# Optimization experiments

Hardware: AMD Instinct MI355X
Metric: run time of the kernel (lower is better)

## Reference

```python
import jax, jax.numpy as jnp
import numpy as np
from jax import lax

LOOKBACK = 336
N_FEATURES = 164
HORIZON = 96
D_MODEL = 64
D_STATE = 16
D_CONV = 4
EXPAND = 2
D_INNER = EXPAND * D_MODEL  # 128
DT_RANK = (D_MODEL + 15) // 16  # 4
MLP_HIDDEN = 64
BATCH = 512


def setup_inputs() -> dict:
    key = jax.random.key(0)
    ks = jax.random.split(key, 20)
    f32 = jnp.float32
    inp = {}
    inp["x_raw"] = jax.random.normal(ks[0], (BATCH, LOOKBACK), f32)
    inp["x_features"] = jax.random.normal(ks[1], (BATCH, N_FEATURES), f32)
    # embed Linear(1, d_model)
    inp["embed_W"] = jax.random.normal(ks[2], (1, D_MODEL), f32) * 0.5
    inp["embed_b"] = jnp.zeros((D_MODEL,), f32)
    # Mamba params (mamba-ssm layout, stored as [in, out] for matmul)
    inp["in_W"] = jax.random.normal(ks[3], (D_MODEL, 2 * D_INNER), f32) * (1.0 / np.sqrt(D_MODEL))
    inp["conv_W"] = jax.random.normal(ks[4], (D_INNER, D_CONV), f32) * 0.3
    inp["conv_b"] = jnp.zeros((D_INNER,), f32)
    inp["xproj_W"] = jax.random.normal(ks[5], (D_INNER, DT_RANK + 2 * D_STATE), f32) * (1.0 / np.sqrt(D_INNER))
    inp["dt_W"] = jax.random.normal(ks[6], (DT_RANK, D_INNER), f32) * (1.0 / np.sqrt(DT_RANK))
    inp["dt_b"] = jax.random.uniform(ks[7], (D_INNER,), f32, -4.0, -2.0)  # softplus -> small dt
    # A_log init = log(arange(1..d_state)) broadcast over d_inner, as in mamba-ssm
    inp["A_log"] = jnp.log(jnp.broadcast_to(jnp.arange(1, D_STATE + 1, dtype=f32), (D_INNER, D_STATE)))
    inp["D"] = jnp.ones((D_INNER,), f32)
    inp["out_W"] = jax.random.normal(ks[8], (D_INNER, D_MODEL), f32) * (1.0 / np.sqrt(D_INNER))
    # MLP stream
    inp["mlp_W1"] = jax.random.normal(ks[9], (N_FEATURES, MLP_HIDDEN), f32) * (1.0 / np.sqrt(N_FEATURES))
    inp["mlp_b1"] = jnp.zeros((MLP_HIDDEN,), f32)
    inp["mlp_W2"] = jax.random.normal(ks[10], (MLP_HIDDEN, MLP_HIDDEN // 2), f32) * (1.0 / np.sqrt(MLP_HIDDEN))
    inp["mlp_b2"] = jnp.zeros((MLP_HIDDEN // 2,), f32)
    # prediction head
    fin = D_MODEL + MLP_HIDDEN // 2
    inp["head_W"] = jax.random.normal(ks[11], (fin, HORIZON), f32) * (1.0 / np.sqrt(fin))
    inp["head_b"] = jnp.zeros((HORIZON,), f32)
    return inp


def silu(x):
    return x * jax.nn.sigmoid(x)


def mamba_block(u, in_W, conv_W, conv_b, xproj_W, dt_W, dt_b, A_log, D, out_W):
    # u: [B, L, d_model]
    B_, L, _ = u.shape
    xz = u @ in_W                      # [B, L, 2*D_INNER]
    x, z = jnp.split(xz, 2, axis=-1)   # each [B, L, D_INNER]
    # causal depthwise conv1d (pad left d_conv-1), then SiLU
    xc = x.transpose(0, 2, 1)          # [B, D_INNER, L]
    kern = conv_W[:, None, :]          # [D_INNER, 1, K] (OIH)
    xc = lax.conv_general_dilated(xc, kern, window_strides=(1,),
                                  padding=[(D_CONV - 1, 0)],
                                  dimension_numbers=("NCH", "OIH", "NCH"),
                                  feature_group_count=D_INNER)
    xc = silu(xc + conv_b[None, :, None])
    x = xc.transpose(0, 2, 1)          # [B, L, D_INNER]
    # input-dependent SSM params
    x_dbl = x @ xproj_W                # [B, L, DT_RANK + 2*D_STATE]
    dt = x_dbl[..., :DT_RANK]
    Bm = x_dbl[..., DT_RANK:DT_RANK + D_STATE]          # [B, L, N]
    Cm = x_dbl[..., DT_RANK + D_STATE:]                 # [B, L, N]
    delta = jax.nn.softplus(dt @ dt_W + dt_b)           # [B, L, D_INNER]
    A = -jnp.exp(A_log)                                 # [D_INNER, N]

    # selective scan over time
    def step(h, inps):
        d_t, B_t, C_t, x_t = inps  # [B,Di], [B,N], [B,N], [B,Di]
        dA = jnp.exp(d_t[:, :, None] * A[None])              # [B, Di, N]
        dBx = (d_t * x_t)[:, :, None] * B_t[:, None, :]      # [B, Di, N]
        h = dA * h + dBx
        y_t = jnp.einsum("bdn,bn->bd", h, C_t)
        return h, y_t

    h0 = jnp.zeros((B_, D_INNER, D_STATE), u.dtype)
    seq = (delta.transpose(1, 0, 2), Bm.transpose(1, 0, 2),
           Cm.transpose(1, 0, 2), x.transpose(1, 0, 2))
    _, ys = lax.scan(step, h0, seq)        # ys: [L, B, D_INNER]
    y = ys.transpose(1, 0, 2) + x * D[None, None, :]
    y = y * silu(z)
    return y @ out_W                        # [B, L, d_model]


def reference(x_raw, x_features, embed_W, embed_b, in_W, conv_W, conv_b,
              xproj_W, dt_W, dt_b, A_log, D, out_W,
              mlp_W1, mlp_b1, mlp_W2, mlp_b2, head_W, head_b):
    # embed raw series: [B, L] -> [B, L, 1] -> [B, L, d_model]
    h = x_raw[..., None] @ embed_W + embed_b
    h = mamba_block(h, in_W, conv_W, conv_b, xproj_W, dt_W, dt_b, A_log, D, out_W)
    h_mamba_out = h[:, -1, :]                       # [B, d_model]
    h_mlp = jax.nn.relu(x_features @ mlp_W1 + mlp_b1) @ mlp_W2 + mlp_b2
    h_final = jnp.concatenate([h_mamba_out, h_mlp], axis=1)
    return h_final @ head_W + head_b                # [B, horizon]
```

## Files before the change

kernel.cpp:

```cpp
#include <hip/hip_runtime.h>
#include <math.h>

#define LOOKBACK 336
#define NFEAT    164
#define HORIZON  96
#define DMODEL   64
#define DSTATE   16
#define DINNER   128
#define MLPH     64
#define BATCH    512
#define XCP      132
#define NG       4
#define GSEG     84
#define CHK      12
#define NCH      7
#define HSTR     20

typedef float v2f __attribute__((ext_vector_type(2)));

__device__ __forceinline__ float fast_rcp(float x) { return __builtin_amdgcn_rcpf(x); }
__device__ __forceinline__ float silu_f(float x) {
    return x * fast_rcp(1.f + __expf(-x));
}

__global__ __launch_bounds__(512, 4) void mamba_one(
    const float* __restrict__ x_raw,   const float* __restrict__ x_features,
    const float* __restrict__ embed_W, const float* __restrict__ embed_b,
    const float* __restrict__ in_W,
    const float* __restrict__ conv_W,  const float* __restrict__ conv_b,
    const float* __restrict__ xproj_W, const float* __restrict__ dt_W,
    const float* __restrict__ dt_b,    const float* __restrict__ A_log,
    const float* __restrict__ Dvec,    const float* __restrict__ out_W,
    const float* __restrict__ mlp_W1,  const float* __restrict__ mlp_b1,
    const float* __restrict__ mlp_W2,  const float* __restrict__ mlp_b2,
    const float* __restrict__ head_W,  const float* __restrict__ head_b,
    float* __restrict__ out)
{
    __shared__ __align__(16) float xrl[344];
    __shared__ __align__(16) float xprojT[20*XCP];
    __shared__ __align__(16) float xcbuf[2][NG][CHK*XCP];
    __shared__ __align__(16) float Bsh[NG][CHK][DSTATE];
    __shared__ __align__(16) float dtraw[NG][CHK][4];
    __shared__ float xcl[DINNER], zsil[DINNER], Cl[DSTATE], yv[DINNER];
    __shared__ float hfin[96], mlph[MLPH];

    const int tid = threadIdx.x;
    const int b   = blockIdx.x;
    const int g   = tid >> 7;
    const int ch  = tid & 127;

    for (int i = tid; i < 339; i += 512)
        xrl[i] = (i >= 3) ? x_raw[b*LOOKBACK + i - 3] : 0.f;
    for (int idx = tid; idx < 20*DINNER; idx += 512) {
        int jj = idx >> 7, d = idx & 127;
        xprojT[jj*XCP + d] = xproj_W[d*36 + jj];
    }

    float w1 = 0.f, w0 = 0.f;
    for (int dm = 0; dm < DMODEL; ++dm) {
        float w = in_W[dm*(2*DINNER) + ch];
        w1 = fmaf(embed_W[dm], w, w1);
        w0 = fmaf(embed_b[dm], w, w0);
    }
    const float4 cw = *(const float4*)&conv_W[ch*4];
    const float  cb = conv_b[ch];
    const float dtw0 = dt_W[ch],       dtw1 = dt_W[128 + ch],
                dtw2 = dt_W[256 + ch], dtw3 = dt_W[384 + ch];
    const float dtb_r = dt_b[ch];
    bool structured = true;
    #pragma unroll
    for (int i = 0; i < 16; ++i) {
        float a = __expf(A_log[ch*DSTATE + i]);
        float ex = (float)(i + 1);
        structured = structured && (fabsf(a - ex) < 1e-3f * ex);
    }
    const bool sfast = __all(structured);

    const int a2jp  = tid / 24;
    const int a2rem = tid - a2jp*24;
    const int a2sub = a2rem / 12;
    const int a2tt  = a2rem - a2sub*12;
    const int cch    = (tid - 256) & 127;
    const int gfirst = (tid - 256) >> 7;
    __syncthreads();

    {
        float* xw = &xcbuf[0][g][0];
        const float* xr = &xrl[g*GSEG];
        if (g == 0) {
            for (int tt = 0; tt < CHK; ++tt) {
                float acc = cb;
                if (tt >= 3) acc = fmaf(fmaf(xr[tt],   w1, w0), cw.x, acc);
                if (tt >= 2) acc = fmaf(fmaf(xr[tt+1], w1, w0), cw.y, acc);
                if (tt >= 1) acc = fmaf(fmaf(xr[tt+2], w1, w0), cw.z, acc);
                acc = fmaf(fmaf(xr[tt+3], w1, w0), cw.w, acc);
                xw[tt*XCP + ch] = silu_f(acc);
            }
        } else {
            float e0 = fmaf(xr[0], w1, w0);
            float e1 = fmaf(xr[1], w1, w0);
            float e2 = fmaf(xr[2], w1, w0);
            #pragma unroll
            for (int tt = 0; tt < CHK; ++tt) {
                float e3 = fmaf(xr[tt+3], w1, w0);
                float acc = cb + e0*cw.x + e1*cw.y + e2*cw.z + e3*cw.w;
                xw[tt*XCP + ch] = silu_f(acc);
                e0 = e1; e1 = e2; e2 = e3;
            }
        }
    }
    __syncthreads();

    v2f h01={0,0},h23={0,0},h45={0,0},h67={0,0},
        h89={0,0},hAB={0,0},hCD={0,0},hEF={0,0};
    float dacc = 0.f;

    for (int c = 0; c < NCH; ++c) {
        const int buf = c & 1;

        if (tid < 240) {
            const int ga = a2sub*2, gb = a2sub*2 + 1;
            const int j0 = a2jp*2;
            const float* p0  = &xprojT[j0*XCP];
            const float* p1  = &xprojT[(j0+1)*XCP];
            const float* xra = &xcbuf[buf][ga][a2tt*XCP];
            const float* xrb = &xcbuf[buf][gb][a2tt*XCP];
            v2f a0a={0,0}, a1a={0,0}, a0b={0,0}, a1b={0,0};
            #pragma unroll 4
            for (int d = 0; d < DINNER; d += 4) {
                float4 q0 = *(const float4*)(p0 + d);
                float4 q1 = *(const float4*)(p1 + d);
                float4 xa = *(const float4*)(xra + d);
                float4 xb = *(const float4*)(xrb + d);
                v2f q0l={q0.x,q0.y}, q0h={q0.z,q0.w};
                v2f q1l={q1.x,q1.y}, q1h={q1.z,q1.w};
                v2f xal={xa.x,xa.y}, xah={xa.z,xa.w};
                v2f xbl={xb.x,xb.y}, xbh={xb.z,xb.w};
                a0a = __builtin_elementwise_fma(xal, q0l, a0a);
                a0a = __builtin_elementwise_fma(xah, q0h, a0a);
                a1a = __builtin_elementwise_fma(xal, q1l, a1a);
                a1a = __builtin_elementwise_fma(xah, q1h, a1a);
                a0b = __builtin_elementwise_fma(xbl, q0l, a0b);
                a0b = __builtin_elementwise_fma(xbh, q0h, a0b);
                a1b = __builtin_elementwise_fma(xbl, q1l, a1b);
                a1b = __builtin_elementwise_fma(xbh, q1h, a1b);
            }
            float r0a=a0a.x+a0a.y, r1a=a1a.x+a1a.y;
            float r0b=a0b.x+a0b.y, r1b=a1b.x+a1b.y;
            if (j0 < 4) {
                *(float2*)&dtraw[ga][a2tt][j0] = make_float2(r0a, r1a);
                *(float2*)&dtraw[gb][a2tt][j0] = make_float2(r0b, r1b);
            } else {
                *(float2*)&Bsh[ga][a2tt][j0-4] = make_float2(r0a, r1a);
                *(float2*)&Bsh[gb][a2tt][j0-4] = make_float2(r0b, r1b);
            }
        } else if (tid >= 256) {
            if (c + 1 < NCH) {
                #pragma unroll
                for (int q = 0; q < 2; ++q) {
                    const int gg = gfirst + q*2;
                    float* xw = &xcbuf[buf^1][gg][0];
                    const float* xr = &xrl[gg*GSEG + (c+1)*CHK];
                    float e0 = fmaf(xr[0], w1, w0);
                    float e1 = fmaf(xr[1], w1, w0);
                    float e2 = fmaf(xr[2], w1, w0);
                    float v = 0.f;
                    #pragma unroll
                    for (int tt = 0; tt < CHK; ++tt) {
                        float e3 = fmaf(xr[tt+3], w1, w0);
                        float acc = cb + e0*cw.x + e1*cw.y + e2*cw.z + e3*cw.w;
                        v = silu_f(acc);
                        xw[tt*XCP + cch] = v;
                        e0 = e1; e1 = e2; e2 = e3;
                    }
                    if (gg == NG-1 && c + 1 == NCH-1) xcl[cch] = v;
                }
            } else {
                if (tid < 384) {
                    const int c2 = tid - 256;
                    float a1 = 0.f, a0 = 0.f;
                    for (int dm = 0; dm < DMODEL; ++dm) {
                        float w = in_W[dm*(2*DINNER) + DINNER + c2];
                        a1 = fmaf(embed_W[dm], w, a1);
                        a0 = fmaf(embed_b[dm], w, a0);
                    }
                    zsil[c2] = silu_f(fmaf(xrl[338], a1, a0));
                } else if (tid < 448) {
                    const int lane = tid - 384;
                    const int n = lane & 15, q = lane >> 4;
                    float acc = 0.f;
                    for (int d = q*32; d < q*32 + 32; ++d)
                        acc = fmaf(xcl[d], xproj_W[d*36 + 20 + n], acc);
                    acc += __shfl_xor(acc, 16);
                    acc += __shfl_xor(acc, 32);
                    if (lane < 16) Cl[n] = acc;
                } else {
                    const int j = tid - 448;
                    const float* xf = x_features + b*NFEAT;
                    float acc = 0.f;
                    for (int f = 0; f < NFEAT; ++f)
                        acc = fmaf(xf[f], mlp_W1[f*MLPH + j], acc);
                    mlph[j] = fmaxf(acc + mlp_b1[j], 0.f);
                }
            }
        }
        __syncthreads();

        const float* xs = &xcbuf[buf][g][0];
        if (__builtin_expect(sfast, 1)) {
            #pragma unroll
            for (int tt = 0; tt < CHK; ++tt) {
                float4 dr = *(const float4*)&dtraw[g][tt][0];
                float dv = fmaf(dr.x, dtw0, fmaf(dr.y, dtw1,
                           fmaf(dr.z, dtw2, fmaf(dr.w, dtw3, dtb_r))));
                float e  = __expf(dv);
                float p  = 1.f + e;
                float r  = fast_rcp(p);
                float dl = (dv > 80.f) ? dv : __logf(p);
                dacc += dl;
                float ux = dl * xs[tt*XCP + ch];
                float4 B0 = *(const float4*)&Bsh[g][tt][0];
                float4 B1 = *(const float4*)&Bsh[g][tt][4];
                float4 B2 = *(const float4*)&Bsh[g][tt][8];
                float4 B3 = *(const float4*)&Bsh[g][tt][12];
                float r2 = r*r, r4 = r2*r2, r8 = r4*r4;
                v2f r2v = {r2, r2}, r4v = {r4, r4}, r8v = {r8, r8};
                v2f p01 = {r, r2};
                v2f p23 = p01*r2v;
                v2f p45 = p01*r4v, p67 = p23*r4v;
                v2f p89 = p01*r8v, pAB = p23*r8v, pCD = p45*r8v, pEF = p67*r8v;
                v2f uxv = {ux, ux};
                h01 = __builtin_elementwise_fma(p01, h01, uxv*(v2f){B0.x,B0.y});
                h23 = __builtin_elementwise_fma(p23, h23, uxv*(v2f){B0.z,B0.w});
                h45 = __builtin_elementwise_fma(p45, h45, uxv*(v2f){B1.x,B1.y});
                h67 = __builtin_elementwise_fma(p67, h67, uxv*(v2f){B1.z,B1.w});
                h89 = __builtin_elementwise_fma(p89, h89, uxv*(v2f){B2.x,B2.y});
                hAB = __builtin_elementwise_fma(pAB, hAB, uxv*(v2f){B2.z,B2.w});
                hCD = __builtin_elementwise_fma(pCD, hCD, uxv*(v2f){B3.x,B3.y});
                hEF = __builtin_elementwise_fma(pEF, hEF, uxv*(v2f){B3.z,B3.w});
            }
        } else {
            const float* Arow = A_log + ch*DSTATE;
            for (int tt = 0; tt < CHK; ++tt) {
                float4 dr = *(const float4*)&dtraw[g][tt][0];
                float dv = fmaf(dr.x, dtw0, fmaf(dr.y, dtw1,
                           fmaf(dr.z, dtw2, fmaf(dr.w, dtw3, dtb_r))));
                float e  = __expf(dv);
                float dl = (dv > 15.f) ? dv : __logf(1.f + e);
                dacc += dl;
                float ux = dl * xs[tt*XCP + ch];
                const float* Brow = &Bsh[g][tt][0];
                float hv[16] = {h01.x,h01.y,h23.x,h23.y,h45.x,h45.y,h67.x,h67.y,
                                h89.x,h89.y,hAB.x,hAB.y,hCD.x,hCD.y,hEF.x,hEF.y};
                for (int i = 0; i < 16; ++i)
                    hv[i] = fmaf(__expf(-__expf(Arow[i])*dl), hv[i], ux*Brow[i]);
                h01=(v2f){hv[0],hv[1]};   h23=(v2f){hv[2],hv[3]};
                h45=(v2f){hv[4],hv[5]};   h67=(v2f){hv[6],hv[7]};
                h89=(v2f){hv[8],hv[9]};   hAB=(v2f){hv[10],hv[11]};
                hCD=(v2f){hv[12],hv[13]}; hEF=(v2f){hv[14],hv[15]};
            }
        }
        __syncthreads();
    }

    float* hpart = &xcbuf[0][0][0];
    float* dsum  = &Bsh[0][0][0];
    {
        float4* hp = (float4*)&hpart[(g*128 + ch)*HSTR];
        hp[0] = make_float4(h01.x,h01.y,h23.x,h23.y);
        hp[1] = make_float4(h45.x,h45.y,h67.x,h67.y);
        hp[2] = make_float4(h89.x,h89.y,hAB.x,hAB.y);
        hp[3] = make_float4(hCD.x,hCD.y,hEF.x,hEF.y);
        dsum[g*128 + ch] = dacc;
    }
    __syncthreads();

    float H[16];
    if (tid < 128) {
        {
            const float4* hp = (const float4*)&hpart[tid*HSTR];
            float4 a = hp[0], bq = hp[1], cq = hp[2], dq = hp[3];
            H[0]=a.x;  H[1]=a.y;  H[2]=a.z;  H[3]=a.w;
            H[4]=bq.x; H[5]=bq.y; H[6]=bq.z; H[7]=bq.w;
            H[8]=cq.x; H[9]=cq.y; H[10]=cq.z;H[11]=cq.w;
            H[12]=dq.x;H[13]=dq.y;H[14]=dq.z;H[15]=dq.w;
        }
        for (int gg = 1; gg < NG; ++gg) {
            float D = dsum[gg*128 + tid];
            const float4* hp = (const float4*)&hpart[(gg*128 + tid)*HSTR];
            float4 a = hp[0], bq = hp[1], cq = hp[2], dq = hp[3];
            float hg[16] = {a.x,a.y,a.z,a.w,bq.x,bq.y,bq.z,bq.w,
                            cq.x,cq.y,cq.z,cq.w,dq.x,dq.y,dq.z,dq.w};
            if (structured) {
                float r = __expf(-D);
                float pw = 1.f;
                #pragma unroll
                for (int i = 0; i < 16; ++i) {
                    pw *= r;
                    H[i] = fmaf(pw, H[i], hg[i]);
                }
            } else {
                #pragma unroll
                for (int i = 0; i < 16; ++i)
                    H[i] = fmaf(__expf(-__expf(A_log[tid*DSTATE+i])*D), H[i], hg[i]);
            }
        }
    }
    __syncthreads();

    if (tid < 128) {
        float acc = 0.f;
        #pragma unroll
        for (int i = 0; i < 16; ++i) acc = fmaf(H[i], Cl[i], acc);
        float y = acc + xcl[tid]*Dvec[tid];
        yv[tid] = y * zsil[tid];
    } else if (tid < 192) {
        const int lane = tid - 128;
        const int j = lane >> 1, k = lane & 1;
        float acc = 0.f;
        for (int kk = k*32; kk < k*32 + 32; ++kk)
            acc = fmaf(mlph[kk], mlp_W2[kk*32 + j], acc);
        acc += __shfl_xor(acc, 1);
        if (k == 0) hfin[64 + j] = acc + mlp_b2[j];
    }
    __syncthreads();

    if (tid < 256) {
        const int o = tid >> 2, k = tid & 3;
        float acc = 0.f;
        for (int d = k*32; d < k*32 + 32; ++d)
            acc = fmaf(yv[d], out_W[d*DMODEL + o], acc);
        acc += __shfl_xor(acc, 1);
        acc += __shfl_xor(acc, 2);
        if (k == 0) hfin[o] = acc;
    }
    __syncthreads();

    if (tid < 192) {
        const int o = tid >> 1, k = tid & 1;
        float acc = 0.f;
        for (int i = k*48; i < k*48 + 48; ++i)
            acc = fmaf(hfin[i], head_W[i*HORIZON + o], acc);
        acc += __shfl_xor(acc, 1);
        if (k == 0) out[b*HORIZON + o] = acc + head_b[o];
    }
}

extern "C" void kernel_launch(void* const* d_in, const int* in_sizes, int n_in,
                              void* d_out, int out_size, void* d_ws, size_t ws_size,
                              hipStream_t stream) {
    (void)in_sizes; (void)n_in; (void)out_size; (void)d_ws; (void)ws_size;
    mamba_one<<<BATCH, 512, 0, stream>>>(
        (const float*)d_in[0],  (const float*)d_in[1],  (const float*)d_in[2],
        (const float*)d_in[3],  (const float*)d_in[4],  (const float*)d_in[5],
        (const float*)d_in[6],  (const float*)d_in[7],  (const float*)d_in[8],
        (const float*)d_in[9],  (const float*)d_in[10], (const float*)d_in[11],
        (const float*)d_in[12], (const float*)d_in[13], (const float*)d_in[14],
        (const float*)d_in[15], (const float*)d_in[16], (const float*)d_in[17],
        (const float*)d_in[18], (float*)d_out);
}
```

Baseline: 191.5 us.

## Split per-batch scan across two 256-thread blocks plus separate epilogue kernel

The single 512-thread-per-batch kernel becomes two launches. First, a scan kernel runs two 256-thread blocks per batch, each covering half the sequence as two chunk groups and writing combined partial states and delta sums to workspace. Second, a 128-thread epilogue kernel merges the two halves and does the C projection, z gate, out projection, MLP and head. This is meant to raise occupancy and parallelism, at the cost of an extra launch and a global workspace round trip.

```diff
diff --git a/kernel.cpp b/kernel.cpp
--- a/kernel.cpp
+++ b/kernel.cpp
@@ -10,11 +10,12 @@
 #define MLPH     64
 #define BATCH    512
 #define XCP      132
-#define NG       4
+#define NGL      2
 #define GSEG     84
 #define CHK      12
 #define NCH      7
 #define HSTR     20
+#define WSB      4480
 
 typedef float v2f __attribute__((ext_vector_type(2)));
 
@@ -23,35 +24,32 @@
     return x * fast_rcp(1.f + __expf(-x));
 }
 
-__global__ __launch_bounds__(512, 4) void mamba_one(
-    const float* __restrict__ x_raw,   const float* __restrict__ x_features,
+__global__ __launch_bounds__(256, 2) void mamba_scan2(
+    const float* __restrict__ x_raw,
     const float* __restrict__ embed_W, const float* __restrict__ embed_b,
     const float* __restrict__ in_W,
     const float* __restrict__ conv_W,  const float* __restrict__ conv_b,
     const float* __restrict__ xproj_W, const float* __restrict__ dt_W,
     const float* __restrict__ dt_b,    const float* __restrict__ A_log,
-    const float* __restrict__ Dvec,    const float* __restrict__ out_W,
-    const float* __restrict__ mlp_W1,  const float* __restrict__ mlp_b1,
-    const float* __restrict__ mlp_W2,  const float* __restrict__ mlp_b2,
-    const float* __restrict__ head_W,  const float* __restrict__ head_b,
-    float* __restrict__ out)
+    float* __restrict__ ws)
 {
-    __shared__ __align__(16) float xrl[344];
+    __shared__ __align__(16) float xrl[172];
     __shared__ __align__(16) float xprojT[20*XCP];
-    __shared__ __align__(16) float xcbuf[2][NG][CHK*XCP];
-    __shared__ __align__(16) float Bsh[NG][CHK][DSTATE];
-    __shared__ __align__(16) float dtraw[NG][CHK][4];
-    __shared__ float xcl[DINNER], zsil[DINNER], Cl[DSTATE], yv[DINNER];
-    __shared__ float hfin[96], mlph[MLPH];
-
-    const int tid = threadIdx.x;
-    const int b   = blockIdx.x;
-    const int g   = tid >> 7;
-    const int ch  = tid & 127;
-
-    for (int i = tid; i < 339; i += 512)
-        xrl[i] = (i >= 3) ? x_raw[b*LOOKBACK + i - 3] : 0.f;
-    for (int idx = tid; idx < 20*DINNER; idx += 512) {
+    __shared__ __align__(16) float xcbuf[2][NGL][CHK*XCP];
+    __shared__ __align__(16) float Bsh[NGL][CHK][DSTATE];
+    __shared__ __align__(16) float dtraw[NGL][CHK][4];
+
+    const int tid   = threadIdx.x;
+    const int batch = blockIdx.x >> 1;
+    const int half  = blockIdx.x & 1;
+    const int gl    = tid >> 7;
+    const int ch    = tid & 127;
+
+    for (int i = tid; i < 171; i += 256) {
+        int t = half*168 + i - 3;
+        xrl[i] = (t >= 0) ? x_raw[batch*LOOKBACK + t] : 0.f;
+    }
+    for (int idx = tid; idx < 20*DINNER; idx += 256) {
         int jj = idx >> 7, d = idx & 127;
         xprojT[jj*XCP + d] = xproj_W[d*36 + jj];
     }
@@ -76,18 +74,15 @@
     }
     const bool sfast = __all(structured);
 
-    const int a2jp  = tid / 24;
-    const int a2rem = tid - a2jp*24;
-    const int a2sub = a2rem / 12;
-    const int a2tt  = a2rem - a2sub*12;
-    const int cch    = (tid - 256) & 127;
-    const int gfirst = (tid - 256) >> 7;
-    __syncthreads();
-
-    {
-        float* xw = &xcbuf[0][g][0];
-        const float* xr = &xrl[g*GSEG];
-        if (g == 0) {
+    const int a2jp = tid / 12;
+    const int a2tt = tid - a2jp*12;
+    const int cch = tid & 127;
+    __syncthreads();
+
+    {
+        float* xw = &xcbuf[0][gl][0];
+        const float* xr = &xrl[gl*GSEG];
+        if (half == 0 && gl == 0) {
             for (int tt = 0; tt < CHK; ++tt) {
                 float acc = cb;
                 if (tt >= 3) acc = fmaf(fmaf(xr[tt],   w1, w0), cw.x, acc);
@@ -118,13 +113,12 @@
     for (int c = 0; c < NCH; ++c) {
         const int buf = c & 1;
 
-        if (tid < 240) {
-            const int ga = a2sub*2, gb = a2sub*2 + 1;
+        if (tid < 120) {
             const int j0 = a2jp*2;
             const float* p0  = &xprojT[j0*XCP];
             const float* p1  = &xprojT[(j0+1)*XCP];
-            const float* xra = &xcbuf[buf][ga][a2tt*XCP];
-            const float* xrb = &xcbuf[buf][gb][a2tt*XCP];
+            const float* xra = &xcbuf[buf][0][a2tt*XCP];
+            const float* xrb = &xcbuf[buf][1][a2tt*XCP];
             v2f a0a={0,0}, a1a={0,0}, a0b={0,0}, a1b={0,0};
             #pragma unroll 4
             for (int d = 0; d < DINNER; d += 4) {
@@ -148,69 +142,40 @@
             float r0a=a0a.x+a0a.y, r1a=a1a.x+a1a.y;
             float r0b=a0b.x+a0b.y, r1b=a1b.x+a1b.y;
             if (j0 < 4) {
-                *(float2*)&dtraw[ga][a2tt][j0] = make_float2(r0a, r1a);
-                *(float2*)&dtraw[gb][a2tt][j0] = make_float2(r0b, r1b);
+                *(float2*)&dtraw[0][a2tt][j0] = make_float2(r0a, r1a);
+                *(float2*)&dtraw[1][a2tt][j0] = make_float2(r0b, r1b);
             } else {
-                *(float2*)&Bsh[ga][a2tt][j0-4] = make_float2(r0a, r1a);
-                *(float2*)&Bsh[gb][a2tt][j0-4] = make_float2(r0b, r1b);
-            }
-        } else if (tid >= 256) {
-            if (c + 1 < NCH) {
+                *(float2*)&Bsh[0][a2tt][j0-4] = make_float2(r0a, r1a);
+                *(float2*)&Bsh[1][a2tt][j0-4] = make_float2(r0b, r1b);
+            }
+        } else if (tid >= 128 && c + 1 < NCH) {
+            #pragma unroll
+            for (int q = 0; q < 2; ++q) {
+                float* xw = &xcbuf[buf^1][q][0];
+                const float* xr = &xrl[q*GSEG + (c+1)*CHK];
+                float e0 = fmaf(xr[0], w1, w0);
+                float e1 = fmaf(xr[1], w1, w0);
+                float e2 = fmaf(xr[2], w1, w0);
+                float v = 0.f;
                 #pragma unroll
-                for (int q = 0; q < 2; ++q) {
-                    const int gg = gfirst + q*2;
-                    float* xw = &xcbuf[buf^1][gg][0];
-                    const float* xr = &xrl[gg*GSEG + (c+1)*CHK];
-                    float e0 = fmaf(xr[0], w1, w0);
-                    float e1 = fmaf(xr[1], w1, w0);
-                    float e2 = fmaf(xr[2], w1, w0);
-                    float v = 0.f;
-                    #pragma unroll
-                    for (int tt = 0; tt < CHK; ++tt) {
-                        float e3 = fmaf(xr[tt+3], w1, w0);
-                        float acc = cb + e0*cw.x + e1*cw.y + e2*cw.z + e3*cw.w;
-                        v = silu_f(acc);
-                        xw[tt*XCP + cch] = v;
-                        e0 = e1; e1 = e2; e2 = e3;
-                    }
-                    if (gg == NG-1 && c + 1 == NCH-1) xcl[cch] = v;
+                for (int tt = 0; tt < CHK; ++tt) {
+                    float e3 = fmaf(xr[tt+3], w1, w0);
+                    float acc = cb + e0*cw.x + e1*cw.y + e2*cw.z + e3*cw.w;
+                    v = silu_f(acc);
+                    xw[tt*XCP + cch] = v;
+                    e0 = e1; e1 = e2; e2 = e3;
                 }
-            } else {
-                if (tid < 384) {
-                    const int c2 = tid - 256;
-                    float a1 = 0.f, a0 = 0.f;
-                    for (int dm = 0; dm < DMODEL; ++dm) {
-                        float w = in_W[dm*(2*DINNER) + DINNER + c2];
-                        a1 = fmaf(embed_W[dm], w, a1);
-                        a0 = fmaf(embed_b[dm], w, a0);
-                    }
-                    zsil[c2] = silu_f(fmaf(xrl[338], a1, a0));
-                } else if (tid < 448) {
-                    const int lane = tid - 384;
-                    const int n = lane & 15, q = lane >> 4;
-                    float acc = 0.f;
-                    for (int d = q*32; d < q*32 + 32; ++d)
-                        acc = fmaf(xcl[d], xproj_W[d*36 + 20 + n], acc);
-                    acc += __shfl_xor(acc, 16);
-                    acc += __shfl_xor(acc, 32);
-                    if (lane < 16) Cl[n] = acc;
-                } else {
-                    const int j = tid - 448;
-                    const float* xf = x_features + b*NFEAT;
-                    float acc = 0.f;
-                    for (int f = 0; f < NFEAT; ++f)
-                        acc = fmaf(xf[f], mlp_W1[f*MLPH + j], acc);
-                    mlph[j] = fmaxf(acc + mlp_b1[j], 0.f);
-                }
+                if (half == 1 && q == 1 && c + 1 == NCH-1)
+                    ws[(size_t)batch*WSB + 4352 + cch] = v;
             }
         }
         __syncthreads();
 
-        const float* xs = &xcbuf[buf][g][0];
+        const float* xs = &xcbuf[buf][gl][0];
         if (__builtin_expect(sfast, 1)) {
             #pragma unroll
             for (int tt = 0; tt < CHK; ++tt) {
-                float4 dr = *(const float4*)&dtraw[g][tt][0];
+                float4 dr = *(const float4*)&dtraw[gl][tt][0];
                 float dv = fmaf(dr.x, dtw0, fmaf(dr.y, dtw1,
                            fmaf(dr.z, dtw2, fmaf(dr.w, dtw3, dtb_r))));
                 float e  = __expf(dv);
@@ -219,10 +184,10 @@
                 float dl = (dv > 80.f) ? dv : __logf(p);
                 dacc += dl;
                 float ux = dl * xs[tt*XCP + ch];
-                float4 B0 = *(const float4*)&Bsh[g][tt][0];
-                float4 B1 = *(const float4*)&Bsh[g][tt][4];
-                float4 B2 = *(const float4*)&Bsh[g][tt][8];
-                float4 B3 = *(const float4*)&Bsh[g][tt][12];
+                float4 B0 = *(const float4*)&Bsh[gl][tt][0];
+                float4 B1 = *(const float4*)&Bsh[gl][tt][4];
+                float4 B2 = *(const float4*)&Bsh[gl][tt][8];
+                float4 B3 = *(const float4*)&Bsh[gl][tt][12];
                 float r2 = r*r, r4 = r2*r2, r8 = r4*r4;
                 v2f r2v = {r2, r2}, r4v = {r4, r4}, r8v = {r8, r8};
                 v2f p01 = {r, r2};
@@ -242,14 +207,14 @@
         } else {
             const float* Arow = A_log + ch*DSTATE;
             for (int tt = 0; tt < CHK; ++tt) {
-                float4 dr = *(const float4*)&dtraw[g][tt][0];
+                float4 dr = *(const float4*)&dtraw[gl][tt][0];
                 float dv = fmaf(dr.x, dtw0, fmaf(dr.y, dtw1,
                            fmaf(dr.z, dtw2, fmaf(dr.w, dtw3, dtb_r))));
                 float e  = __expf(dv);
                 float dl = (dv > 15.f) ? dv : __logf(1.f + e);
                 dacc += dl;
                 float ux = dl * xs[tt*XCP + ch];
-                const float* Brow = &Bsh[g][tt][0];
+                const float* Brow = &Bsh[gl][tt][0];
                 float hv[16] = {h01.x,h01.y,h23.x,h23.y,h45.x,h45.y,h67.x,h67.y,
                                 h89.x,h89.y,hAB.x,hAB.y,hCD.x,hCD.y,hEF.x,hEF.y};
                 for (int i = 0; i < 16; ++i)
@@ -265,58 +230,151 @@
 
     float* hpart = &xcbuf[0][0][0];
     float* dsum  = &Bsh[0][0][0];
-    {
-        float4* hp = (float4*)&hpart[(g*128 + ch)*HSTR];
+    if (gl == 0) {
+        float4* hp = (float4*)&hpart[ch*HSTR];
         hp[0] = make_float4(h01.x,h01.y,h23.x,h23.y);
         hp[1] = make_float4(h45.x,h45.y,h67.x,h67.y);
         hp[2] = make_float4(h89.x,h89.y,hAB.x,hAB.y);
         hp[3] = make_float4(hCD.x,hCD.y,hEF.x,hEF.y);
-        dsum[g*128 + ch] = dacc;
-    }
-    __syncthreads();
+        dsum[ch] = dacc;
+    }
+    __syncthreads();
+    if (gl == 1) {
+        const float4* hp = (const float4*)&hpart[ch*HSTR];
+        float4 a = hp[0], bq = hp[1], cq = hp[2], dq = hp[3];
+        float h0[16] = {a.x,a.y,a.z,a.w,bq.x,bq.y,bq.z,bq.w,
+                        cq.x,cq.y,cq.z,cq.w,dq.x,dq.y,dq.z,dq.w};
+        float h1[16] = {h01.x,h01.y,h23.x,h23.y,h45.x,h45.y,h67.x,h67.y,
+                        h89.x,h89.y,hAB.x,hAB.y,hCD.x,hCD.y,hEF.x,hEF.y};
+        float P[16];
+        if (structured) {
+            float r = __expf(-dacc);
+            float pw = 1.f;
+            #pragma unroll
+            for (int i = 0; i < 16; ++i) { pw *= r; P[i] = fmaf(pw, h0[i], h1[i]); }
+        } else {
+            #pragma unroll
+            for (int i = 0; i < 16; ++i)
+                P[i] = fmaf(__expf(-__expf(A_log[ch*DSTATE+i])*dacc), h0[i], h1[i]);
+        }
+        float* wsb = ws + (size_t)batch*WSB + half*2176;
+        float4* pw4 = (float4*)(wsb + ch*16);
+        pw4[0] = make_float4(P[0],P[1],P[2],P[3]);
+        pw4[1] = make_float4(P[4],P[5],P[6],P[7]);
+        pw4[2] = make_float4(P[8],P[9],P[10],P[11]);
+        pw4[3] = make_float4(P[12],P[13],P[14],P[15]);
+        wsb[2048 + ch] = dsum[ch] + dacc;
+    }
+}
+
+__global__ __launch_bounds__(128, 2) void mamba_epi(
+    const float* __restrict__ x_raw,   const float* __restrict__ x_features,
+    const float* __restrict__ embed_W, const float* __restrict__ embed_b,
+    const float* __restrict__ in_W,    const float* __restrict__ xproj_W,
+    const float* __restrict__ A_log,   const float* __restrict__ Dvec,
+    const float* __restrict__ out_W,
+    const float* __restrict__ mlp_W1,  const float* __restrict__ mlp_b1,
+    const float* __restrict__ mlp_W2,  const float* __restrict__ mlp_b2,
+    const float* __restrict__ head_W,  const float* __restrict__ head_b,
+    const float* __restrict__ ws,      float* __restrict__ out)
+{
+    __shared__ float xcl[DINNER], Cpart[8][16], Cl[DSTATE], yv[DINNER];
+    __shared__ float hfin[96], mlph[MLPH];
+
+    const int ch = threadIdx.x;
+    const int b  = blockIdx.x;
+    const float* wsb = ws + (size_t)b*WSB;
+
+    xcl[ch] = wsb[4352 + ch];
+
+    bool structured = true;
+    #pragma unroll
+    for (int i = 0; i < 16; ++i) {
+        float a = __expf(A_log[ch*DSTATE + i]);
+        float ex = (float)(i + 1);
+        structured = structured && (fabsf(a - ex) < 1e-3f * ex);
+    }
 
     float H[16];
-    if (tid < 128) {
-        {
-            const float4* hp = (const float4*)&hpart[tid*HSTR];
-            float4 a = hp[0], bq = hp[1], cq = hp[2], dq = hp[3];
-            H[0]=a.x;  H[1]=a.y;  H[2]=a.z;  H[3]=a.w;
-            H[4]=bq.x; H[5]=bq.y; H[6]=bq.z; H[7]=bq.w;
-            H[8]=cq.x; H[9]=cq.y; H[10]=cq.z;H[11]=cq.w;
-            H[12]=dq.x;H[13]=dq.y;H[14]=dq.z;H[15]=dq.w;
-        }
-        for (int gg = 1; gg < NG; ++gg) {
-            float D = dsum[gg*128 + tid];
-            const float4* hp = (const float4*)&hpart[(gg*128 + tid)*HSTR];
-            float4 a = hp[0], bq = hp[1], cq = hp[2], dq = hp[3];
-            float hg[16] = {a.x,a.y,a.z,a.w,bq.x,bq.y,bq.z,bq.w,
-                            cq.x,cq.y,cq.z,cq.w,dq.x,dq.y,dq.z,dq.w};
-            if (structured) {
-                float r = __expf(-D);
-                float pw = 1.f;
-                #pragma unroll
-                for (int i = 0; i < 16; ++i) {
-                    pw *= r;
-                    H[i] = fmaf(pw, H[i], hg[i]);
-                }
-            } else {
-                #pragma unroll
-                for (int i = 0; i < 16; ++i)
-                    H[i] = fmaf(__expf(-__expf(A_log[tid*DSTATE+i])*D), H[i], hg[i]);
-            }
-        }
-    }
-    __syncthreads();
-
-    if (tid < 128) {
+    {
+        const float4* p01 = (const float4*)(wsb + ch*16);
+        const float4* p23 = (const float4*)(wsb + 2176 + ch*16);
+        float D23 = wsb[2176 + 2048 + ch];
+        float4 a0 = p01[0], a1 = p01[1], a2 = p01[2], a3 = p01[3];
+        float4 b0 = p23[0], b1 = p23[1], b2 = p23[2], b3 = p23[3];
+        float P0[16] = {a0.x,a0.y,a0.z,a0.w,a1.x,a1.y,a1.z,a1.w,
+                        a2.x,a2.y,a2.z,a2.w,a3.x,a3.y,a3.z,a3.w};
+        float P1[16] = {b0.x,b0.y,b0.z,b0.w,b1.x,b1.y,b1.z,b1.w,
+                        b2.x,b2.y,b2.z,b2.w,b3.x,b3.y,b3.z,b3.w};
+        if (structured) {
+            float r = __expf(-D23);
+            float pw = 1.f;
+            #pragma unroll
+            for (int i = 0; i < 16; ++i) { pw *= r; H[i] = fmaf(pw, P0[i], P1[i]); }
+        } else {
+            #pragma unroll
+            for (int i = 0; i < 16; ++i)
+                H[i] = fmaf(__expf(-__expf(A_log[ch*DSTATE+i])*D23), P0[i], P1[i]);
+        }
+    }
+
+    float zs;
+    {
+        float a1 = 0.f, a0 = 0.f;
+        for (int dm = 0; dm < DMODEL; ++dm) {
+            float w = in_W[dm*(2*DINNER) + DINNER + ch];
+            a1 = fmaf(embed_W[dm], w, a1);
+            a0 = fmaf(embed_b[dm], w, a0);
+        }
+        zs = silu_f(fmaf(x_raw[b*LOOKBACK + 335], a1, a0));
+    }
+    __syncthreads();
+
+    {
+        const int q = ch >> 4, n = ch & 15;
+        float acc = 0.f;
+        for (int d = q*16; d < q*16 + 16; ++d)
+            acc = fmaf(xcl[d], xproj_W[d*36 + 20 + n], acc);
+        Cpart[q][n] = acc;
+    }
+    __syncthreads();
+
+    if (ch < 16) {
+        float s = 0.f;
+        #pragma unroll
+        for (int q = 0; q < 8; ++q) s += Cpart[q][ch];
+        Cl[ch] = s;
+    } else if (ch >= 64) {
+        const int j = ch - 64;
+        const float* xf = x_features + b*NFEAT;
+        float acc = 0.f;
+        for (int f = 0; f < NFEAT; ++f)
+            acc = fmaf(xf[f], mlp_W1[f*MLPH + j], acc);
+        mlph[j] = fmaxf(acc + mlp_b1[j], 0.f);
+    }
+    __syncthreads();
+
+    {
         float acc = 0.f;
         #pragma unroll
         for (int i = 0; i < 16; ++i) acc = fmaf(H[i], Cl[i], acc);
-        float y = acc + xcl[tid]*Dvec[tid];
-        yv[tid] = y * zsil[tid];
-    } else if (tid < 192) {
-        const int lane = tid - 128;
-        const int j = lane >> 1, k = lane & 1;
+        float y = acc + xcl[ch]*Dvec[ch];
+        yv[ch] = y * zs;
+    }
+    __syncthreads();
+
+    {
+        const int o = ch >> 1, k = ch & 1;
+        float acc = 0.f;
+        for (int d = k*64; d < k*64 + 64; ++d)
+            acc = fmaf(yv[d], out_W[d*DMODEL + o], acc);
+        acc += __shfl_xor(acc, 1);
+        if (k == 0) hfin[o] = acc;
+    }
+    __syncthreads();
+
+    if (ch < 64) {
+        const int j = ch >> 1, k = ch & 1;
         float acc = 0.f;
         for (int kk = k*32; kk < k*32 + 32; ++kk)
             acc = fmaf(mlph[kk], mlp_W2[kk*32 + j], acc);
@@ -325,37 +383,30 @@
     }
     __syncthreads();
 
-    if (tid < 256) {
-        const int o = tid >> 2, k = tid & 3;
-        float acc = 0.f;
-        for (int d = k*32; d < k*32 + 32; ++d)
-            acc = fmaf(yv[d], out_W[d*DMODEL + o], acc);
-        acc += __shfl_xor(acc, 1);
-        acc += __shfl_xor(acc, 2);
-        if (k == 0) hfin[o] = acc;
-    }
-    __syncthreads();
-
-    if (tid < 192) {
-        const int o = tid >> 1, k = tid & 1;
-        float acc = 0.f;
-        for (int i = k*48; i < k*48 + 48; ++i)
-            acc = fmaf(hfin[i], head_W[i*HORIZON + o], acc);
-        acc += __shfl_xor(acc, 1);
-        if (k == 0) out[b*HORIZON + o] = acc + head_b[o];
+    if (ch < HORIZON) {
+        float acc = 0.f;
+        for (int i = 0; i < 96; ++i)
+            acc = fmaf(hfin[i], head_W[i*HORIZON + ch], acc);
+        out[b*HORIZON + ch] = acc + head_b[ch];
     }
 }
 
 extern "C" void kernel_launch(void* const* d_in, const int* in_sizes, int n_in,
                               void* d_out, int out_size, void* d_ws, size_t ws_size,
                               hipStream_t stream) {
-    (void)in_sizes; (void)n_in; (void)out_size; (void)d_ws; (void)ws_size;
-    mamba_one<<<BATCH, 512, 0, stream>>>(
+    (void)in_sizes; (void)n_in; (void)out_size; (void)ws_size;
+    float* ws = (float*)d_ws;
+    mamba_scan2<<<BATCH*2, 256, 0, stream>>>(
+        (const float*)d_in[0],
+        (const float*)d_in[2],  (const float*)d_in[3],  (const float*)d_in[4],
+        (const float*)d_in[5],  (const float*)d_in[6],  (const float*)d_in[7],
+        (const float*)d_in[8],  (const float*)d_in[9],  (const float*)d_in[10],
+        ws);
+    mamba_epi<<<BATCH, 128, 0, stream>>>(
         (const float*)d_in[0],  (const float*)d_in[1],  (const float*)d_in[2],
-        (const float*)d_in[3],  (const float*)d_in[4],  (const float*)d_in[5],
-        (const float*)d_in[6],  (const float*)d_in[7],  (const float*)d_in[8],
-        (const float*)d_in[9],  (const float*)d_in[10], (const float*)d_in[11],
-        (const float*)d_in[12], (const float*)d_in[13], (const float*)d_in[14],
-        (const float*)d_in[15], (const float*)d_in[16], (const float*)d_in[17],
-        (const float*)d_in[18], (float*)d_out);
+        (const float*)d_in[3],  (const float*)d_in[4],  (const float*)d_in[7],
+        (const float*)d_in[10], (const float*)d_in[11], (const float*)d_in[12],
+        (const float*)d_in[13], (const float*)d_in[14], (const float*)d_in[15],
+        (const float*)d_in[16], (const float*)d_in[17], (const float*)d_in[18],
+        ws, (float*)d_out);
 }
```

Result: faster. 176.3 us (-7.9%).
